# Performance work log

Hardware: AMD Instinct MI355X
Metric: run time of the kernel (lower is better)

## Reference

```python
import jax, jax.numpy as jnp
import numpy as np

B, S, A, M = 131072, 376, 17, 5
H1, H2 = 400, 300
LOG_STD_MIN, LOG_STD_MAX = -10.0, 2.0
EPIS_MIN, EPIS_MAX = 4.53999297624848e-05, 7.38905609893065


def _uniform(k, shape, fan_in):
    bound = 1.0 / np.sqrt(fan_in)
    return jax.random.uniform(k, shape, jnp.float32, -bound, bound)


def setup_inputs() -> dict:
    key = jax.random.key(0)
    ks = jax.random.split(key, 8)
    W1 = _uniform(ks[0], (S, H1), S); b1 = _uniform(ks[1], (H1,), S)
    W2 = _uniform(ks[2], (H1, H2), H1); b2 = _uniform(ks[3], (H2,), H1)
    W3 = _uniform(ks[4], (H2, A * M * 3), H2); b3 = _uniform(ks[5], (A * M * 3,), H2)
    state = jax.random.normal(ks[6], (B, S), jnp.float32)
    eps = jax.random.normal(ks[7], (B, A), jnp.float32)
    return {"state": state, "eps": eps, "W1": W1, "b1": b1, "W2": W2, "b2": b2, "W3": W3, "b3": b3}


def _mixture_stats(state, W1, b1, W2, b2, W3, b3):
    h = jax.nn.relu(state @ W1 + b1)
    h = jax.nn.relu(h @ W2 + b2)
    out = jnp.tanh(h @ W3 + b3)                      # [B, 3*A*M]
    mw, mm, lms = jnp.split(out, 3, axis=-1)
    mw = mw.reshape(-1, A, M)
    mm = mm.reshape(-1, A, M)
    lms = lms.reshape(-1, A, M)
    w = jax.nn.softmax(mw, axis=2)                   # max-subtraction is built in
    std = jnp.exp(jnp.clip(lms, LOG_STD_MIN, LOG_STD_MAX))
    mean = jnp.sum(w * mm, axis=2)                   # [B, A]
    alea = jnp.sum(w * std, axis=2)
    epis = jnp.sum(w * jnp.square(mm - mean[:, :, None]), axis=2)
    epis = jnp.clip(epis, EPIS_MIN, EPIS_MAX)
    return mean, alea + epis, epis


def _diag_logprob(x, mean, std):
    # MVN with covariance diag(std^2) == independent diagonal Gaussian
    z = (x - mean) / std
    d = x.shape[-1]
    return -0.5 * jnp.sum(z * z + 2.0 * jnp.log(std), axis=-1) - 0.5 * d * jnp.log(2.0 * jnp.pi).astype(x.dtype)


def reference(state, eps, W1, b1, W2, b2, W3, b3):
    mean, total, epis = _mixture_stats(state, W1, b1, W2, b2, W3, b3)
    sample = mean + total * eps                      # rsample of N(mean, diag(total^2))
    tanh_sample = jnp.tanh(sample)
    lp_ttl = _diag_logprob(sample, mean, total)
    lp_eps = _diag_logprob(sample, mean, epis)
    corr = jnp.sum(jnp.log(1.0 - jnp.square(tanh_sample) + 1e-6), axis=1, keepdims=True)
    log_pi_ttl = lp_ttl[:, None] - corr
    log_pi_eps = lp_eps[:, None] - corr
    return tanh_sample, log_pi_ttl, log_pi_eps
```

## Files before the change

kernel.cpp:

```cpp
#include <hip/hip_runtime.h>

typedef _Float16 half8 __attribute__((ext_vector_type(8)));
typedef float floatx4 __attribute__((ext_vector_type(4)));

#define BATCH 131072
#define S_DIM 376
#define NACT 17

#define L1_NT 28
#define L1_CH 12
#define L2_NT 20
#define L2_CH 13
#define L3_NT 16
#define L3_CH 10
#define L1F 0
#define L2F (L1_NT * L1_CH * 1024)
#define L3F (L2F + L2_NT * L2_CH * 1024)
#define WTOTF (L3F + L3_NT * L3_CH * 1024)

#define ROWS 32
#define AW1 416
#define AW2 328
#define OW3 260
#define BRING_OFF 53248
#define LDS_BYTES (53248 + 4 * 3 * 2048)

#define MFMA16(a, b, c) __builtin_amdgcn_mfma_f32_16x16x32_f16(a, b, c, 0, 0, 0)

__global__ __launch_bounds__(256) void prep_kernel(const float* __restrict__ W1,
                                                   const float* __restrict__ W2,
                                                   const float* __restrict__ W3,
                                                   _Float16* __restrict__ ws) {
  int idx = blockIdx.x * 256 + threadIdx.x;
  if (idx >= WTOTF) return;
  const float* W;
  int CH, NR, KR, e = idx;
  if (e < L2F) {
    W = W1; CH = L1_CH; NR = 400; KR = 376;
  } else if (e < L3F) {
    W = W2; CH = L2_CH; NR = 300; KR = 400; e -= L2F;
  } else {
    W = W3; CH = L3_CH; NR = 255; KR = 300; e -= L3F;
  }
  const int f = e >> 10, r = e & 1023;
  const int plane = r >> 9, rr = r & 511;
  const int lane = rr >> 3, j = rr & 7;
  const int q = lane >> 4, m = lane & 15;
  const int ntile = f / CH, kc = f - ntile * CH;
  const int n = ntile * 16 + m, k = kc * 32 + q * 8 + j;
  const float v = (n < NR && k < KR) ? W[k * NR + n] : 0.f;
  const _Float16 hi = (_Float16)v;
  ws[idx] = plane ? (_Float16)(v - (float)hi) : hi;
}

__device__ __forceinline__ void dma16(const _Float16* g, char* l) {
  __builtin_amdgcn_global_load_lds(
      (const __attribute__((address_space(1))) void*)g,
      (__attribute__((address_space(3))) void*)l, 16, 0, 0);
}
template <int W>
__device__ __forceinline__ void wait_vm() {
  if constexpr (W >= 4) asm volatile("s_waitcnt vmcnt(4)" ::: "memory");
  else if constexpr (W == 2) asm volatile("s_waitcnt vmcnt(2)" ::: "memory");
  else asm volatile("s_waitcnt vmcnt(0)" ::: "memory");
}
__device__ __forceinline__ void wait_lgkm0() {
  asm volatile("s_waitcnt lgkmcnt(0)" ::: "memory");
}

template <int AW, bool SWZ>
__device__ __forceinline__ half8 lds_frag(const char* base, int row, int koff) {
  int off = (row * AW + koff) * 2;
  if (SWZ) off ^= (row & 7) << 4;
  return *(const half8*)(base + off);
}

template <int NT, int CHUNKS, int AW, bool SWZ, int I>
struct KStep {
  static constexpr int TOT = NT * CHUNKS;
  static __device__ __forceinline__ void run(const char* Ahi, const char* Alo,
                                             const _Float16* bbg, char* bring,
                                             int lane16, int m, int kq,
                                             half8 (&bh)[2], half8 (&bl)[2],
                                             half8 (&ah)[2], half8 (&al)[2],
                                             half8 (&ahn)[2], half8 (&aln)[2],
                                             floatx4 (&acc)[2][NT]) {
    constexpr int nt = I % NT;
    constexpr int kc = I / NT;
    constexpr int cs = I & 1, ns = cs ^ 1;
    acc[0][nt] = MFMA16(ah[0], bh[cs], acc[0][nt]);
    acc[1][nt] = MFMA16(ah[1], bh[cs], acc[1][nt]);
    acc[0][nt] = MFMA16(ah[0], bl[cs], acc[0][nt]);
    __builtin_amdgcn_sched_barrier(0);
    if constexpr (I + 3 < TOT) {
      wait_lgkm0();
      constexpr int fo = (((I + 3) % NT) * CHUNKS + ((I + 3) / NT)) * 1024;
      char* dslot = bring + (I % 3) * 2048;
      dma16(bbg + fo, dslot);
      dma16(bbg + fo + 512, dslot + 1024);
    }
    __builtin_amdgcn_sched_barrier(0);
    acc[1][nt] = MFMA16(ah[1], bl[cs], acc[1][nt]);
    acc[0][nt] = MFMA16(al[0], bh[cs], acc[0][nt]);
    acc[1][nt] = MFMA16(al[1], bh[cs], acc[1][nt]);
    __builtin_amdgcn_sched_barrier(0);
    if constexpr (I + 1 < TOT) {
      constexpr int JMAX = (I + 3 < TOT) ? (I + 3) : (TOT - 1);
      constexpr int WN = 2 * (JMAX - (I + 1));
      wait_vm<WN>();
      const char* slot = (const char*)bring + ((I + 1) % 3) * 2048;
      bh[ns] = *(const half8*)(slot + lane16);
      bl[ns] = *(const half8*)(slot + 1024 + lane16);
    }
    if constexpr (nt == NT - 2 && kc + 1 < CHUNKS) {
      ahn[0] = lds_frag<AW, SWZ>(Ahi, m, (kc + 1) * 32 + kq);
      ahn[1] = lds_frag<AW, SWZ>(Ahi, 16 + m, (kc + 1) * 32 + kq);
      aln[0] = lds_frag<AW, SWZ>(Alo, m, (kc + 1) * 32 + kq);
      aln[1] = lds_frag<AW, SWZ>(Alo, 16 + m, (kc + 1) * 32 + kq);
    }
    if constexpr (nt == NT - 1 && kc + 1 < CHUNKS) {
      ah[0] = ahn[0]; ah[1] = ahn[1]; al[0] = aln[0]; al[1] = aln[1];
    }
    if constexpr (I + 1 < TOT)
      KStep<NT, CHUNKS, AW, SWZ, I + 1>::run(Ahi, Alo, bbg, bring, lane16, m, kq,
                                             bh, bl, ah, al, ahn, aln, acc);
  }
};

template <int NT, int CHUNKS, int AW, bool SWZ>
__device__ __forceinline__ void gemm_layer(const _Float16* __restrict__ Ahi_,
                                           const _Float16* __restrict__ Alo_,
                                           const _Float16* __restrict__ Bf,
                                           char* bring,
                                           int ntile0, int lane, int q, int m,
                                           floatx4 (&acc)[2][NT]) {
  const char* Ahi = (const char*)Ahi_;
  const char* Alo = (const char*)Alo_;
  const int kq = q * 8;
  const int lane16 = lane * 16;
  const _Float16* bbg = Bf + ntile0 * CHUNKS * 1024 + lane * 8;

  half8 bh[2], bl[2];
  half8 ah[2], al[2], ahn[2], aln[2];

#pragma unroll
  for (int s = 0; s < 3; ++s) {
    dma16(bbg + s * CHUNKS * 1024, bring + s * 2048);
    dma16(bbg + s * CHUNKS * 1024 + 512, bring + s * 2048 + 1024);
  }
  ah[0] = lds_frag<AW, SWZ>(Ahi, m, kq);
  ah[1] = lds_frag<AW, SWZ>(Ahi, 16 + m, kq);
  al[0] = lds_frag<AW, SWZ>(Alo, m, kq);
  al[1] = lds_frag<AW, SWZ>(Alo, 16 + m, kq);
  wait_vm<4>();
  bh[0] = *(const half8*)((const char*)bring + lane16);
  bl[0] = *(const half8*)((const char*)bring + 1024 + lane16);
  __builtin_amdgcn_sched_barrier(0);

  KStep<NT, CHUNKS, AW, SWZ, 0>::run(Ahi, Alo, bbg, bring, lane16, m, kq,
                                     bh, bl, ah, al, ahn, aln, acc);
}

__global__ __launch_bounds__(256) void actor_kernel(const float* __restrict__ state,
                                                    const float* __restrict__ eps,
                                                    const float* __restrict__ b1,
                                                    const float* __restrict__ b2,
                                                    const float* __restrict__ b3,
                                                    const _Float16* __restrict__ wsp,
                                                    float* __restrict__ out) {
  extern __shared__ char smem[];
  _Float16* Ahi = (_Float16*)smem;
  _Float16* Alo = Ahi + ROWS * AW1;

  const int t = threadIdx.x;
  const int wave = t >> 6;
  const int lane = t & 63;
  const int q = lane >> 4;
  const int m = lane & 15;
  char* bring = smem + BRING_OFF + wave * (3 * 2048);
  const long rowbase = (long)blockIdx.x * ROWS;

  {
    const int row = t >> 3, p = t & 7;
    const long gbase = (rowbase + row) * S_DIM;
#pragma unroll
    for (int c0 = 0; c0 < 6; ++c0) {
      const int col = c0 * 64 + p * 8;
      float v[8];
      if (col + 8 <= S_DIM) {
        const float4* sp = (const float4*)(state + gbase + col);
        float4 x0 = sp[0], x1 = sp[1];
        v[0] = x0.x; v[1] = x0.y; v[2] = x0.z; v[3] = x0.w;
        v[4] = x1.x; v[5] = x1.y; v[6] = x1.z; v[7] = x1.w;
      } else {
#pragma unroll
        for (int j = 0; j < 8; ++j) v[j] = 0.f;
      }
      half8 h, l;
#pragma unroll
      for (int j = 0; j < 8; ++j) {
        _Float16 hi = (_Float16)v[j];
        h[j] = hi;
        l[j] = (_Float16)(v[j] - (float)hi);
      }
      int off = (row * AW1 + col) * 2;
      off ^= (row & 7) << 4;
      *(half8*)((char*)Ahi + off) = h;
      *(half8*)((char*)Alo + off) = l;
    }
  }
  __syncthreads();

  floatx4 acc1[2][7];
#pragma unroll
  for (int a = 0; a < 2; ++a)
#pragma unroll
    for (int b = 0; b < 7; ++b) { acc1[a][b][0] = 0.f; acc1[a][b][1] = 0.f; acc1[a][b][2] = 0.f; acc1[a][b][3] = 0.f; }
  gemm_layer<7, 12, AW1, true>(Ahi, Alo, wsp + L1F, bring, wave * 7, lane, q, m, acc1);

  __syncthreads();
  _Float16* H1hi = Ahi;
  _Float16* H1lo = Alo;
#pragma unroll
  for (int nt = 0; nt < 7; ++nt) {
    const int tile = wave * 7 + nt;
    if (tile < 26) {
      const int col = tile * 16 + m;
      const float bias = (col < 400) ? b1[col] : 0.f;
#pragma unroll
      for (int mt = 0; mt < 2; ++mt)
#pragma unroll
        for (int r = 0; r < 4; ++r) {
          const int row = mt * 16 + q * 4 + r;
          float v = fmaxf(acc1[mt][nt][r] + bias, 0.f);
          _Float16 hi = (_Float16)v;
          int off = (row * AW1 + col) * 2;
          off ^= (row & 7) << 4;
          *(_Float16*)((char*)H1hi + off) = hi;
          *(_Float16*)((char*)H1lo + off) = (_Float16)(v - (float)hi);
        }
    }
  }
  __syncthreads();

  floatx4 acc2[2][5];
#pragma unroll
  for (int a = 0; a < 2; ++a)
#pragma unroll
    for (int b = 0; b < 5; ++b) { acc2[a][b][0] = 0.f; acc2[a][b][1] = 0.f; acc2[a][b][2] = 0.f; acc2[a][b][3] = 0.f; }
  gemm_layer<5, 13, AW1, true>(H1hi, H1lo, wsp + L2F, bring, wave * 5, lane, q, m, acc2);

  __syncthreads();
  _Float16* H2hi = (_Float16*)smem;
  _Float16* H2lo = H2hi + ROWS * AW2;
#pragma unroll
  for (int nt = 0; nt < 5; ++nt) {
    const int col = (wave * 5 + nt) * 16 + m;
    const float bias = (col < 300) ? b2[col] : 0.f;
#pragma unroll
    for (int mt = 0; mt < 2; ++mt)
#pragma unroll
      for (int r = 0; r < 4; ++r) {
        const int row = mt * 16 + q * 4 + r;
        float v = fmaxf(acc2[mt][nt][r] + bias, 0.f);
        _Float16 hi = (_Float16)v;
        H2hi[row * AW2 + col] = hi;
        H2lo[row * AW2 + col] = (_Float16)(v - (float)hi);
      }
  }
  __syncthreads();

  floatx4 acc3[2][4];
#pragma unroll
  for (int a = 0; a < 2; ++a)
#pragma unroll
    for (int b = 0; b < 4; ++b) { acc3[a][b][0] = 0.f; acc3[a][b][1] = 0.f; acc3[a][b][2] = 0.f; acc3[a][b][3] = 0.f; }
  gemm_layer<4, 10, AW2, false>(H2hi, H2lo, wsp + L3F, bring, wave * 4, lane, q, m, acc3);

  __syncthreads();
  float* O3 = (float*)smem;
#pragma unroll
  for (int nt = 0; nt < 4; ++nt) {
    const int col = (wave * 4 + nt) * 16 + m;
    const float bias = (col < 255) ? b3[col] : 0.f;
#pragma unroll
    for (int mt = 0; mt < 2; ++mt)
#pragma unroll
      for (int r = 0; r < 4; ++r) {
        const int row = mt * 16 + q * 4 + r;
        O3[row * OW3 + col] = tanhf(acc3[mt][nt][r] + bias);
      }
  }
  __syncthreads();

  {
    const int row = t >> 3, p = t & 7;
    const long gr = rowbase + row;
    const float* Or = O3 + row * OW3;
    float pc = 0.f, pt = 0.f, pe = 0.f;
    const int nact = (p == 0) ? 3 : 2;
    for (int ia = 0; ia < nact; ++ia) {
      const int a = p + ia * 8;
      float mw[5], mmv[5], lms[5];
#pragma unroll
      for (int j = 0; j < 5; ++j) {
        mw[j]  = Or[a * 5 + j];
        mmv[j] = Or[85 + a * 5 + j];
        lms[j] = Or[170 + a * 5 + j];
      }
      float w[5], es = 0.f;
#pragma unroll
      for (int j = 0; j < 5; ++j) { w[j] = expf(mw[j]); es += w[j]; }
      const float inv = 1.f / es;
      float mean = 0.f;
#pragma unroll
      for (int j = 0; j < 5; ++j) { w[j] *= inv; mean += w[j] * mmv[j]; }
      float alea = 0.f, epis = 0.f;
#pragma unroll
      for (int j = 0; j < 5; ++j) {
        float sd = expf(fminf(fmaxf(lms[j], -10.f), 2.f));
        alea += w[j] * sd;
        float d = mmv[j] - mean;
        epis += w[j] * d * d;
      }
      epis = fminf(fmaxf(epis, 4.53999297624848e-05f), 7.38905609893065f);
      const float total = alea + epis;
      const float ea = eps[gr * NACT + a];
      const float sample = mean + total * ea;
      const float ts = tanhf(sample);
      out[gr * NACT + a] = ts;
      pc += logf(1.f - ts * ts + 1e-6f);
      const float dz = sample - mean;
      const float zt = dz / total;
      const float ze = dz / epis;
      pt += zt * zt + 2.f * logf(total);
      pe += ze * ze + 2.f * logf(epis);
    }
    pc += __shfl_xor(pc, 1); pc += __shfl_xor(pc, 2); pc += __shfl_xor(pc, 4);
    pt += __shfl_xor(pt, 1); pt += __shfl_xor(pt, 2); pt += __shfl_xor(pt, 4);
    pe += __shfl_xor(pe, 1); pe += __shfl_xor(pe, 2); pe += __shfl_xor(pe, 4);
    if (p == 0) {
      const float hdl2pi = 15.62195506447944f;
      out[(long)NACT * BATCH + gr] = (-0.5f * pt - hdl2pi) - pc;
      out[(long)(NACT + 1) * BATCH + gr] = (-0.5f * pe - hdl2pi) - pc;
    }
  }
}

extern "C" void kernel_launch(void* const* d_in, const int* in_sizes, int n_in,
                              void* d_out, int out_size, void* d_ws, size_t ws_size,
                              hipStream_t stream) {
  const float* state = (const float*)d_in[0];
  const float* eps   = (const float*)d_in[1];
  const float* W1    = (const float*)d_in[2];
  const float* b1    = (const float*)d_in[3];
  const float* W2    = (const float*)d_in[4];
  const float* b2    = (const float*)d_in[5];
  const float* W3    = (const float*)d_in[6];
  const float* b3    = (const float*)d_in[7];
  float* out = (float*)d_out;
  _Float16* ws = (_Float16*)d_ws;

  (void)in_sizes; (void)n_in; (void)out_size; (void)ws_size;

  hipFuncSetAttribute(reinterpret_cast<const void*>(actor_kernel),
                      hipFuncAttributeMaxDynamicSharedMemorySize, LDS_BYTES);

  prep_kernel<<<(WTOTF + 255) / 256, 256, 0, stream>>>(W1, W2, W3, ws);
  actor_kernel<<<BATCH / ROWS, 256, LDS_BYTES, stream>>>(state, eps, b1, b2, b3, ws, out);
}
```

Baseline: 583.6 us.

## Double rows per block to 64 to reuse each weight fragment across four M-tiles

Raises the batch rows per workgroup from 32 to 64, so each streamed B (weight) fragment feeds four 16-row MFMA tiles instead of two. This halves weight traffic per row and the DMA/wait overhead per MFMA. The state load, the epilogues and the final mixture stage are remapped to four threads per row. In exchange it doubles accumulator and A-fragment registers and LDS use, which risks spills and lower occupancy. The grid has half as many blocks.

```diff
diff --git a/kernel.cpp b/kernel.cpp
--- a/kernel.cpp
+++ b/kernel.cpp
@@ -18,12 +18,12 @@
 #define L3F (L2F + L2_NT * L2_CH * 1024)
 #define WTOTF (L3F + L3_NT * L3_CH * 1024)
 
-#define ROWS 32
+#define ROWS 64
 #define AW1 416
 #define AW2 328
 #define OW3 260
-#define BRING_OFF 53248
-#define LDS_BYTES (53248 + 4 * 3 * 2048)
+#define BRING_OFF (2 * ROWS * AW1 * 2)
+#define LDS_BYTES (BRING_OFF + 4 * 3 * 2048)
 
 #define MFMA16(a, b, c) __builtin_amdgcn_mfma_f32_16x16x32_f16(a, b, c, 0, 0, 0)
 
@@ -82,15 +82,18 @@
                                              const _Float16* bbg, char* bring,
                                              int lane16, int m, int kq,
                                              half8 (&bh)[2], half8 (&bl)[2],
-                                             half8 (&ah)[2], half8 (&al)[2],
-                                             half8 (&ahn)[2], half8 (&aln)[2],
-                                             floatx4 (&acc)[2][NT]) {
+                                             half8 (&ah)[4], half8 (&al)[4],
+                                             half8 (&ahn)[4], half8 (&aln)[4],
+                                             floatx4 (&acc)[4][NT]) {
     constexpr int nt = I % NT;
     constexpr int kc = I / NT;
     constexpr int cs = I & 1, ns = cs ^ 1;
     acc[0][nt] = MFMA16(ah[0], bh[cs], acc[0][nt]);
     acc[1][nt] = MFMA16(ah[1], bh[cs], acc[1][nt]);
+    acc[2][nt] = MFMA16(ah[2], bh[cs], acc[2][nt]);
+    acc[3][nt] = MFMA16(ah[3], bh[cs], acc[3][nt]);
     acc[0][nt] = MFMA16(ah[0], bl[cs], acc[0][nt]);
+    acc[1][nt] = MFMA16(ah[1], bl[cs], acc[1][nt]);
     __builtin_amdgcn_sched_barrier(0);
     if constexpr (I + 3 < TOT) {
       wait_lgkm0();
@@ -100,9 +103,12 @@
       dma16(bbg + fo + 512, dslot + 1024);
     }
     __builtin_amdgcn_sched_barrier(0);
-    acc[1][nt] = MFMA16(ah[1], bl[cs], acc[1][nt]);
+    acc[2][nt] = MFMA16(ah[2], bl[cs], acc[2][nt]);
+    acc[3][nt] = MFMA16(ah[3], bl[cs], acc[3][nt]);
     acc[0][nt] = MFMA16(al[0], bh[cs], acc[0][nt]);
     acc[1][nt] = MFMA16(al[1], bh[cs], acc[1][nt]);
+    acc[2][nt] = MFMA16(al[2], bh[cs], acc[2][nt]);
+    acc[3][nt] = MFMA16(al[3], bh[cs], acc[3][nt]);
     __builtin_amdgcn_sched_barrier(0);
     if constexpr (I + 1 < TOT) {
       constexpr int JMAX = (I + 3 < TOT) ? (I + 3) : (TOT - 1);
@@ -113,13 +119,15 @@
       bl[ns] = *(const half8*)(slot + 1024 + lane16);
     }
     if constexpr (nt == NT - 2 && kc + 1 < CHUNKS) {
-      ahn[0] = lds_frag<AW, SWZ>(Ahi, m, (kc + 1) * 32 + kq);
-      ahn[1] = lds_frag<AW, SWZ>(Ahi, 16 + m, (kc + 1) * 32 + kq);
-      aln[0] = lds_frag<AW, SWZ>(Alo, m, (kc + 1) * 32 + kq);
-      aln[1] = lds_frag<AW, SWZ>(Alo, 16 + m, (kc + 1) * 32 + kq);
+#pragma unroll
+      for (int mt = 0; mt < 4; ++mt) {
+        ahn[mt] = lds_frag<AW, SWZ>(Ahi, mt * 16 + m, (kc + 1) * 32 + kq);
+        aln[mt] = lds_frag<AW, SWZ>(Alo, mt * 16 + m, (kc + 1) * 32 + kq);
+      }
     }
     if constexpr (nt == NT - 1 && kc + 1 < CHUNKS) {
-      ah[0] = ahn[0]; ah[1] = ahn[1]; al[0] = aln[0]; al[1] = aln[1];
+#pragma unroll
+      for (int mt = 0; mt < 4; ++mt) { ah[mt] = ahn[mt]; al[mt] = aln[mt]; }
     }
     if constexpr (I + 1 < TOT)
       KStep<NT, CHUNKS, AW, SWZ, I + 1>::run(Ahi, Alo, bbg, bring, lane16, m, kq,
@@ -133,7 +141,7 @@
                                            const _Float16* __restrict__ Bf,
                                            char* bring,
                                            int ntile0, int lane, int q, int m,
-                                           floatx4 (&acc)[2][NT]) {
+                                           floatx4 (&acc)[4][NT]) {
   const char* Ahi = (const char*)Ahi_;
   const char* Alo = (const char*)Alo_;
   const int kq = q * 8;
@@ -141,17 +149,18 @@
   const _Float16* bbg = Bf + ntile0 * CHUNKS * 1024 + lane * 8;
 
   half8 bh[2], bl[2];
-  half8 ah[2], al[2], ahn[2], aln[2];
+  half8 ah[4], al[4], ahn[4], aln[4];
 
 #pragma unroll
   for (int s = 0; s < 3; ++s) {
     dma16(bbg + s * CHUNKS * 1024, bring + s * 2048);
     dma16(bbg + s * CHUNKS * 1024 + 512, bring + s * 2048 + 1024);
   }
-  ah[0] = lds_frag<AW, SWZ>(Ahi, m, kq);
-  ah[1] = lds_frag<AW, SWZ>(Ahi, 16 + m, kq);
-  al[0] = lds_frag<AW, SWZ>(Alo, m, kq);
-  al[1] = lds_frag<AW, SWZ>(Alo, 16 + m, kq);
+#pragma unroll
+  for (int mt = 0; mt < 4; ++mt) {
+    ah[mt] = lds_frag<AW, SWZ>(Ahi, mt * 16 + m, kq);
+    al[mt] = lds_frag<AW, SWZ>(Alo, mt * 16 + m, kq);
+  }
   wait_vm<4>();
   bh[0] = *(const half8*)((const char*)bring + lane16);
   bl[0] = *(const half8*)((const char*)bring + 1024 + lane16);
@@ -181,11 +190,11 @@
   const long rowbase = (long)blockIdx.x * ROWS;
 
   {
-    const int row = t >> 3, p = t & 7;
+    const int row = t >> 2, p = t & 3;
     const long gbase = (rowbase + row) * S_DIM;
 #pragma unroll
-    for (int c0 = 0; c0 < 6; ++c0) {
-      const int col = c0 * 64 + p * 8;
+    for (int c0 = 0; c0 < 12; ++c0) {
+      const int col = c0 * 32 + p * 8;
       float v[8];
       if (col + 8 <= S_DIM) {
         const float4* sp = (const float4*)(state + gbase + col);
@@ -211,9 +220,9 @@
   }
   __syncthreads();
 
-  floatx4 acc1[2][7];
-#pragma unroll
-  for (int a = 0; a < 2; ++a)
+  floatx4 acc1[4][7];
+#pragma unroll
+  for (int a = 0; a < 4; ++a)
 #pragma unroll
     for (int b = 0; b < 7; ++b) { acc1[a][b][0] = 0.f; acc1[a][b][1] = 0.f; acc1[a][b][2] = 0.f; acc1[a][b][3] = 0.f; }
   gemm_layer<7, 12, AW1, true>(Ahi, Alo, wsp + L1F, bring, wave * 7, lane, q, m, acc1);
@@ -228,7 +237,7 @@
       const int col = tile * 16 + m;
       const float bias = (col < 400) ? b1[col] : 0.f;
 #pragma unroll
-      for (int mt = 0; mt < 2; ++mt)
+      for (int mt = 0; mt < 4; ++mt)
 #pragma unroll
         for (int r = 0; r < 4; ++r) {
           const int row = mt * 16 + q * 4 + r;
@@ -243,9 +252,9 @@
   }
   __syncthreads();
 
-  floatx4 acc2[2][5];
-#pragma unroll
-  for (int a = 0; a < 2; ++a)
+  floatx4 acc2[4][5];
+#pragma unroll
+  for (int a = 0; a < 4; ++a)
 #pragma unroll
     for (int b = 0; b < 5; ++b) { acc2[a][b][0] = 0.f; acc2[a][b][1] = 0.f; acc2[a][b][2] = 0.f; acc2[a][b][3] = 0.f; }
   gemm_layer<5, 13, AW1, true>(H1hi, H1lo, wsp + L2F, bring, wave * 5, lane, q, m, acc2);
@@ -258,7 +267,7 @@
     const int col = (wave * 5 + nt) * 16 + m;
     const float bias = (col < 300) ? b2[col] : 0.f;
 #pragma unroll
-    for (int mt = 0; mt < 2; ++mt)
+    for (int mt = 0; mt < 4; ++mt)
 #pragma unroll
       for (int r = 0; r < 4; ++r) {
         const int row = mt * 16 + q * 4 + r;
@@ -270,9 +279,9 @@
   }
   __syncthreads();
 
-  floatx4 acc3[2][4];
-#pragma unroll
-  for (int a = 0; a < 2; ++a)
+  floatx4 acc3[4][4];
+#pragma unroll
+  for (int a = 0; a < 4; ++a)
 #pragma unroll
     for (int b = 0; b < 4; ++b) { acc3[a][b][0] = 0.f; acc3[a][b][1] = 0.f; acc3[a][b][2] = 0.f; acc3[a][b][3] = 0.f; }
   gemm_layer<4, 10, AW2, false>(H2hi, H2lo, wsp + L3F, bring, wave * 4, lane, q, m, acc3);
@@ -284,7 +293,7 @@
     const int col = (wave * 4 + nt) * 16 + m;
     const float bias = (col < 255) ? b3[col] : 0.f;
 #pragma unroll
-    for (int mt = 0; mt < 2; ++mt)
+    for (int mt = 0; mt < 4; ++mt)
 #pragma unroll
       for (int r = 0; r < 4; ++r) {
         const int row = mt * 16 + q * 4 + r;
@@ -294,13 +303,13 @@
   __syncthreads();
 
   {
-    const int row = t >> 3, p = t & 7;
+    const int row = t >> 2, p = t & 3;
     const long gr = rowbase + row;
     const float* Or = O3 + row * OW3;
     float pc = 0.f, pt = 0.f, pe = 0.f;
-    const int nact = (p == 0) ? 3 : 2;
+    const int nact = (p == 0) ? 5 : 4;
     for (int ia = 0; ia < nact; ++ia) {
-      const int a = p + ia * 8;
+      const int a = p + ia * 4;
       float mw[5], mmv[5], lms[5];
 #pragma unroll
       for (int j = 0; j < 5; ++j) {
@@ -336,9 +345,9 @@
       pt += zt * zt + 2.f * logf(total);
       pe += ze * ze + 2.f * logf(epis);
     }
-    pc += __shfl_xor(pc, 1); pc += __shfl_xor(pc, 2); pc += __shfl_xor(pc, 4);
-    pt += __shfl_xor(pt, 1); pt += __shfl_xor(pt, 2); pt += __shfl_xor(pt, 4);
-    pe += __shfl_xor(pe, 1); pe += __shfl_xor(pe, 2); pe += __shfl_xor(pe, 4);
+    pc += __shfl_xor(pc, 1); pc += __shfl_xor(pc, 2);
+    pt += __shfl_xor(pt, 1); pt += __shfl_xor(pt, 2);
+    pe += __shfl_xor(pe, 1); pe += __shfl_xor(pe, 2);
     if (p == 0) {
       const float hdl2pi = 15.62195506447944f;
       out[(long)NACT * BATCH + gr] = (-0.5f * pt - hdl2pi) - pc;
```

Result: slower. 617.6 us (+5.8%).
